# Kernel optimization log

Measured on AMD Instinct MI355X. Metric: run time of the kernel, lower is better.

Reference implementation:

```python
import jax, jax.numpy as jnp
import numpy as np


def setup_inputs() -> dict:
    key = jax.random.key(0)
    k1, k2 = jax.random.split(key)
    B, Q, K, H = 8, 2048, 2048, 128
    out_state = jax.random.normal(k1, (B, Q, H), dtype=jnp.float32)
    history = jax.random.normal(k2, (B, K, H), dtype=jnp.float32)
    return {"out_state": out_state, "history": history}


def reference(out_state, history):
    # tanh pre-activation on queries
    q = jnp.tanh(out_state)                              # [B, Q, H]
    # unscaled QK^T scores
    scores = jnp.einsum("bqh,bkh->bqk", q, history)      # [B, Q, K]
    probs = jax.nn.softmax(scores, axis=2)               # softmax over keys
    attn = jnp.einsum("bqk,bkh->bqh", probs, history)    # [B, Q, H]
    return attn
```

## Files before the change

### kernel.cpp

```cpp
#include <hip/hip_runtime.h>
#include <math.h>


typedef _Float16 half8 __attribute__((ext_vector_type(8)));
typedef _Float16 half4 __attribute__((ext_vector_type(4)));
typedef float    f32x4 __attribute__((ext_vector_type(4)));

#define QQ 2048
#define KK 2048
#define HH 128
#define BM 64
#define BN 64
#define NTILES 32
#define PS_STR 72
#define L2E 1.44269504f
#define SPLITS_TARGET 3

#define KS_STRP 136
#define VT_STRP 72

#define KH_HALVES     ((size_t)8 * KK * HH)
#define PREP_BYTES    (KH_HALVES * 4)
#define OSPLIT_BYTES  ((size_t)256 * BM * HH * 2)
#define MLSPLIT_FLOATS ((size_t)256 * BM)

union U32H { unsigned int u; _Float16 h[2]; };

typedef __attribute__((address_space(1))) const void gvoid;
typedef __attribute__((address_space(3))) void lvoid;

#define WAITVM4 asm volatile("s_waitcnt vmcnt(4)" ::: "memory")
#define WAITVM0 asm volatile("s_waitcnt vmcnt(0)" ::: "memory")
static __device__ __forceinline__ void wgbar() {
    asm volatile("" ::: "memory");
    __builtin_amdgcn_s_barrier();
    asm volatile("" ::: "memory");
}

__launch_bounds__(256)
__global__ void attn_prep(const float* __restrict__ history,
                          _Float16* __restrict__ wsh) {
    __shared__ __align__(16) _Float16 Ks[BN * KS_STRP];
    __shared__ __align__(16) _Float16 Vt[HH * VT_STRP];

    const int tid = threadIdx.x;
    const int bid = blockIdx.x;
    const int b   = bid >> 5;
    const int kt  = bid & 31;

    const float* hb = history + ((size_t)b * KK + (size_t)kt * BN) * HH;
    const int r0 = tid >> 5;
    const int c4 = (tid & 31) * 4;
    #pragma unroll
    for (int j = 0; j < 8; ++j) {
        const float4 g = *(const float4*)(hb + (size_t)(r0 + 8 * j) * HH + c4);
        half4 hv;
        hv[0] = (_Float16)g.x; hv[1] = (_Float16)g.y;
        hv[2] = (_Float16)g.z; hv[3] = (_Float16)g.w;
        *(half4*)&Ks[(r0 + 8 * j) * KS_STRP + c4] = hv;
    }
    __syncthreads();

    {
        const int h0  = 2 * (tid & 63);
        const int n0t = (tid >> 6) * 16;
        half8 ra0, ra1, rb0, rb1;
        #pragma unroll
        for (int i = 0; i < 8; ++i) {
            U32H t; t.u = *(const unsigned int*)&Ks[(n0t + i) * KS_STRP + h0];
            ra0[i] = t.h[0]; rb0[i] = t.h[1];
        }
        #pragma unroll
        for (int i = 8; i < 16; ++i) {
            U32H t; t.u = *(const unsigned int*)&Ks[(n0t + i) * KS_STRP + h0];
            ra1[i - 8] = t.h[0]; rb1[i - 8] = t.h[1];
        }
        *(half8*)&Vt[(h0    ) * VT_STRP + n0t    ] = ra0;
        *(half8*)&Vt[(h0    ) * VT_STRP + n0t + 8] = ra1;
        *(half8*)&Vt[(h0 + 1) * VT_STRP + n0t    ] = rb0;
        *(half8*)&Vt[(h0 + 1) * VT_STRP + n0t + 8] = rb1;
    }

    {
        const int k  = tid >> 2;
        const int c0 = (tid & 3) * 32;
        const int sk = (k & 7) << 3;
        _Float16* dst = wsh + ((size_t)b * KK + (size_t)kt * BN + k) * HH;
        #pragma unroll
        for (int g8 = 0; g8 < 4; ++g8)
            *(half8*)&dst[(c0 + 8 * g8) ^ sk] = *(const half8*)&Ks[k * KS_STRP + c0 + 8 * g8];
    }
    __syncthreads();

    {
        const int h  = tid >> 1;
        const int n0 = (tid & 1) * 32;
        const int th = (h & 7) << 3;
        _Float16* dst = wsh + KH_HALVES + (((size_t)b * NTILES + kt) * HH + h) * BN;
        #pragma unroll
        for (int g8 = 0; g8 < 4; ++g8)
            *(half8*)&dst[(n0 + 8 * g8) ^ th] = *(const half8*)&Vt[h * VT_STRP + n0 + 8 * g8];
    }
}

__launch_bounds__(256, 3)
__global__ void attn_main(const float* __restrict__ out_state,
                          const _Float16* __restrict__ wsh,
                          float* __restrict__ out,
                          char* __restrict__ wsb,
                          int splits) {
    __shared__ __align__(16) _Float16 Ks[BN * HH];
    __shared__ __align__(16) _Float16 Vt[HH * BN];
    __shared__ __align__(16) _Float16 Ps[4][16 * PS_STR];

    const int tid  = threadIdx.x;
    const int wave = tid >> 6;
    const int lane = tid & 63;
    const int quad = lane >> 4;
    const int lc   = lane & 15;
    const int swz  = (lc & 7) << 3;

    const int bid  = blockIdx.x;
    const int s    = bid >> 8;
    const int r256 = bid & 255;
    const int b    = r256 >> 5;
    const int qb   = r256 & 31;
    const int m0   = qb * BM;

    const int kt0 = (NTILES * s) / splits;
    const int kt1 = (NTILES * (s + 1)) / splits;

    const _Float16* khb = wsh + (size_t)b * KK * HH;
    const _Float16* vtb = wsh + KH_HALVES + (size_t)b * NTILES * (HH * BN);

    auto issueK = [&](int t) {
        const char* gsrc = (const char*)(khb + (size_t)t * (BN * HH));
        #pragma unroll
        for (int c = 0; c < 4; ++c) {
            const int off = (c * 4 + wave) * 1024 + lane * 16;
            __builtin_amdgcn_global_load_lds((gvoid*)(gsrc + off),
                                             (lvoid*)((char*)Ks + off), 16, 0, 0);
        }
    };
    auto issueV = [&](int t) {
        const char* gsrc = (const char*)(vtb + (size_t)t * (HH * BN));
        #pragma unroll
        for (int c = 0; c < 4; ++c) {
            const int off = (c * 4 + wave) * 1024 + lane * 16;
            __builtin_amdgcn_global_load_lds((gvoid*)(gsrc + off),
                                             (lvoid*)((char*)Vt + off), 16, 0, 0);
        }
    };

    issueK(kt0);
    issueV(kt0);

    half8 qf[4];
    {
        const int m = m0 + wave * 16 + lc;
        const float* qrow = out_state + ((size_t)b * QQ + m) * HH;
        float4 qa[8];
        #pragma unroll
        for (int s4 = 0; s4 < 4; ++s4) {
            qa[2 * s4]     = *(const float4*)(qrow + 32 * s4 + quad * 8);
            qa[2 * s4 + 1] = *(const float4*)(qrow + 32 * s4 + quad * 8 + 4);
        }
        #pragma unroll
        for (int s4 = 0; s4 < 4; ++s4) {
            qf[s4][0] = (_Float16)tanhf(qa[2*s4].x);   qf[s4][1] = (_Float16)tanhf(qa[2*s4].y);
            qf[s4][2] = (_Float16)tanhf(qa[2*s4].z);   qf[s4][3] = (_Float16)tanhf(qa[2*s4].w);
            qf[s4][4] = (_Float16)tanhf(qa[2*s4+1].x); qf[s4][5] = (_Float16)tanhf(qa[2*s4+1].y);
            qf[s4][6] = (_Float16)tanhf(qa[2*s4+1].z); qf[s4][7] = (_Float16)tanhf(qa[2*s4+1].w);
        }
    }

    const f32x4 zero4 = {0.f, 0.f, 0.f, 0.f};
    f32x4 O[8];
    #pragma unroll
    for (int i = 0; i < 8; ++i) O[i] = zero4;
    f32x4 Osum = zero4;
    float rmax = -3.0e38f;

    const half8 ones = {(_Float16)1.f,(_Float16)1.f,(_Float16)1.f,(_Float16)1.f,
                        (_Float16)1.f,(_Float16)1.f,(_Float16)1.f,(_Float16)1.f};

    for (int kt = kt0; kt < kt1; ++kt) {
        const bool more = (kt + 1 < kt1);

        WAITVM4;
        wgbar();

        f32x4 S[4];
        __builtin_amdgcn_s_setprio(1);
        #pragma unroll
        for (int nt = 0; nt < 4; ++nt) {
            f32x4 acc = zero4;
            #pragma unroll
            for (int s4 = 0; s4 < 4; ++s4) {
                const half8 kf = *(const half8*)
                    &Ks[((nt * 16 + lc) << 7) + ((32 * s4 + (quad << 3)) ^ swz)];
                acc = __builtin_amdgcn_mfma_f32_16x16x32_f16(kf, qf[s4], acc, 0, 0, 0);
            }
            S[nt] = acc;
        }
        __builtin_amdgcn_s_setprio(0);

        wgbar();
        if (more) issueK(kt + 1);

        float tmax = S[0][0];
        #pragma unroll
        for (int nt = 0; nt < 4; ++nt)
            #pragma unroll
            for (int r = 0; r < 4; ++r)
                tmax = fmaxf(tmax, S[nt][r]);
        tmax = fmaxf(tmax, __shfl_xor(tmax, 16, 64));
        tmax = fmaxf(tmax, __shfl_xor(tmax, 32, 64));

        if (!__all(tmax <= rmax)) {
            const float nm    = fmaxf(rmax, tmax);
            const float alpha = exp2f((rmax - nm) * L2E);
            rmax = nm;
            #pragma unroll
            for (int ct = 0; ct < 8; ++ct) O[ct] *= alpha;
            Osum *= alpha;
        }

        #pragma unroll
        for (int nt = 0; nt < 4; ++nt)
            #pragma unroll
            for (int r = 0; r < 4; ++r)
                S[nt][r] = exp2f((S[nt][r] - rmax) * L2E);

        #pragma unroll
        for (int nt = 0; nt < 4; ++nt) {
            half4 pv;
            pv[0] = (_Float16)S[nt][0]; pv[1] = (_Float16)S[nt][1];
            pv[2] = (_Float16)S[nt][2]; pv[3] = (_Float16)S[nt][3];
            *(half4*)&Ps[wave][lc * PS_STR + nt * 16 + quad * 4] = pv;
        }

        if (more) { WAITVM4; } else { WAITVM0; }
        wgbar();

        __builtin_amdgcn_s_setprio(1);
        #pragma unroll
        for (int s2 = 0; s2 < 2; ++s2) {
            const half8 pb = *(const half8*)&Ps[wave][lc * PS_STR + s2 * 32 + quad * 8];
            Osum = __builtin_amdgcn_mfma_f32_16x16x32_f16(ones, pb, Osum, 0, 0, 0);
            #pragma unroll
            for (int ct = 0; ct < 8; ++ct) {
                const half8 vf = *(const half8*)
                    &Vt[((ct * 16 + lc) << 6) + ((32 * s2 + (quad << 3)) ^ swz)];
                O[ct] = __builtin_amdgcn_mfma_f32_16x16x32_f16(vf, pb, O[ct], 0, 0, 0);
            }
        }
        __builtin_amdgcn_s_setprio(0);

        wgbar();
        if (more) issueV(kt + 1);
    }

    if (splits == 1) {
        const float inv = 1.0f / Osum[0];
        float* orow = out + ((size_t)b * QQ + m0 + wave * 16 + lc) * HH;
        #pragma unroll
        for (int ct = 0; ct < 8; ++ct) {
            f32x4 v = O[ct] * inv;
            *(f32x4*)&orow[ct * 16 + quad * 4] = v;
        }
    } else {
        const float inv = 1.0f / Osum[0];
        _Float16* oh = (_Float16*)(wsb + PREP_BYTES)
                     + ((size_t)(s * 256 + r256) * BM + wave * 16 + lc) * HH;
        #pragma unroll
        for (int ct = 0; ct < 8; ++ct) {
            const f32x4 v = O[ct] * inv;
            half4 hv;
            hv[0] = (_Float16)v[0]; hv[1] = (_Float16)v[1];
            hv[2] = (_Float16)v[2]; hv[3] = (_Float16)v[3];
            *(half4*)&oh[ct * 16 + quad * 4] = hv;
        }
        if (quad == 0) {
            float* wm = (float*)(wsb + PREP_BYTES + (size_t)splits * OSPLIT_BYTES);
            const size_t idx = (size_t)(s * 256 + r256) * BM + wave * 16 + lc;
            wm[idx] = rmax;
            wm[(size_t)splits * MLSPLIT_FLOATS + idx] = Osum[0];
        }
    }
}

__launch_bounds__(256)
__global__ void attn_combine(const char* __restrict__ wsb,
                             float* __restrict__ out,
                             int splits) {
    const int idx = blockIdx.x * 256 + threadIdx.x;
    const int h   = idx & 127;
    const int q   = (idx >> 7) & 2047;
    const int b   = idx >> 18;
    const int qb  = q >> 6;
    const int qr  = q & 63;
    const int blk = b * 32 + qb;

    const _Float16* oh = (const _Float16*)(wsb + PREP_BYTES);
    const float* wm = (const float*)(wsb + PREP_BYTES + (size_t)splits * OSPLIT_BYTES);
    const float* wl = wm + (size_t)splits * MLSPLIT_FLOATS;

    float ms[SPLITS_TARGET];
    float M = -3.0e38f;
    for (int s = 0; s < splits; ++s) {
        ms[s] = wm[(size_t)(s * 256 + blk) * BM + qr];
        M = fmaxf(M, ms[s]);
    }
    float denom = 0.f, val = 0.f;
    for (int s = 0; s < splits; ++s) {
        const float wgt = exp2f((ms[s] - M) * L2E) * wl[(size_t)(s * 256 + blk) * BM + qr];
        denom += wgt;
        val   += wgt * (float)oh[(size_t)(s * 256 + blk) * (BM * HH) + (size_t)qr * HH + h];
    }
    out[idx] = val / denom;
}

extern "C" void kernel_launch(void* const* d_in, const int* in_sizes, int n_in,
                              void* d_out, int out_size, void* d_ws, size_t ws_size,
                              hipStream_t stream) {
    const float* out_state = (const float*)d_in[0];
    const float* history   = (const float*)d_in[1];
    float* out = (float*)d_out;
    char* wsb  = (char*)d_ws;

    const size_t need3 = PREP_BYTES
                       + (size_t)SPLITS_TARGET * OSPLIT_BYTES
                       + (size_t)SPLITS_TARGET * 2 * MLSPLIT_FLOATS * 4;
    const int splits = (ws_size >= need3) ? SPLITS_TARGET : 1;

    attn_prep<<<dim3(256), dim3(256), 0, stream>>>(history, (_Float16*)wsb);
    attn_main<<<dim3(256 * splits), dim3(256), 0, stream>>>(out_state, (const _Float16*)wsb,
                                                            out, wsb, splits);
    if (splits > 1)
        attn_combine<<<dim3((8 * QQ * HH) / 256), dim3(256), 0, stream>>>(wsb, out, splits);
}
```

Before: 120.9 us.

## Switch attention to 32x32 MFMA with register-resident P and four splits

The main kernel moves from 16x16x32 to 32x32x16 MFMA tiles with 2 waves per block, each wave owning 32 query rows. P now stays in registers and is rearranged with cross-half shuffles rather than going through LDS, and the row sum is accumulated with scalar adds instead of a ones-MFMA. tanh and exp use fast hardware exp2/rcp intrinsics. The prep kernel swizzles in LDS and writes coalesced. Splits go to 4 when the workspace allows, and the combine kernel is templated and vectorised. The cost is larger per-thread register pressure and fewer threads per block.

Result: faster. 108.5 us (-10.3%).

```diff
diff --git a/kernel.cpp b/kernel.cpp
--- a/kernel.cpp
+++ b/kernel.cpp
@@ -2,9 +2,12 @@
 #include <math.h>
 
 
-typedef _Float16 half8 __attribute__((ext_vector_type(8)));
-typedef _Float16 half4 __attribute__((ext_vector_type(4)));
-typedef float    f32x4 __attribute__((ext_vector_type(4)));
+typedef _Float16 half8  __attribute__((ext_vector_type(8)));
+typedef _Float16 half4  __attribute__((ext_vector_type(4)));
+typedef __fp16   fp16x2 __attribute__((ext_vector_type(2)));
+typedef float    f32x4  __attribute__((ext_vector_type(4)));
+typedef float    f32x2  __attribute__((ext_vector_type(2)));
+typedef float    f32x16 __attribute__((ext_vector_type(16)));
 
 #define QQ 2048
 #define KK 2048
@@ -12,24 +15,21 @@
 #define BM 64
 #define BN 64
 #define NTILES 32
-#define PS_STR 72
 #define L2E 1.44269504f
-#define SPLITS_TARGET 3
-
-#define KS_STRP 136
-#define VT_STRP 72
-
-#define KH_HALVES     ((size_t)8 * KK * HH)
-#define PREP_BYTES    (KH_HALVES * 4)
-#define OSPLIT_BYTES  ((size_t)256 * BM * HH * 2)
+
+#define KH_HALVES      ((size_t)8 * KK * HH)
+#define PREP_BYTES     (KH_HALVES * 4)
+#define OSPLIT_BYTES   ((size_t)256 * BM * HH * 2)
 #define MLSPLIT_FLOATS ((size_t)256 * BM)
 
 union U32H { unsigned int u; _Float16 h[2]; };
+union H2I  { fp16x2 h; int i; };
+union I4H8 { int i[4]; half8 h; };
 
 typedef __attribute__((address_space(1))) const void gvoid;
 typedef __attribute__((address_space(3))) void lvoid;
 
-#define WAITVM4 asm volatile("s_waitcnt vmcnt(4)" ::: "memory")
+#define WAITVM8 asm volatile("s_waitcnt vmcnt(8)" ::: "memory")
 #define WAITVM0 asm volatile("s_waitcnt vmcnt(0)" ::: "memory")
 static __device__ __forceinline__ void wgbar() {
     asm volatile("" ::: "memory");
@@ -38,10 +38,10 @@
 }
 
 __launch_bounds__(256)
-__global__ void attn_prep(const float* __restrict__ history,
-                          _Float16* __restrict__ wsh) {
-    __shared__ __align__(16) _Float16 Ks[BN * KS_STRP];
-    __shared__ __align__(16) _Float16 Vt[HH * VT_STRP];
+__global__ void attn_prep_k(const float* __restrict__ history,
+                            _Float16* __restrict__ wsh) {
+    __shared__ __align__(16) _Float16 Ks[BN * HH];
+    __shared__ __align__(16) _Float16 Vt[HH * BN];
 
     const int tid = threadIdx.x;
     const int bid = blockIdx.x;
@@ -53,11 +53,12 @@
     const int c4 = (tid & 31) * 4;
     #pragma unroll
     for (int j = 0; j < 8; ++j) {
-        const float4 g = *(const float4*)(hb + (size_t)(r0 + 8 * j) * HH + c4);
+        const int k = r0 + 8 * j;
+        const float4 g = *(const float4*)(hb + (size_t)k * HH + c4);
         half4 hv;
         hv[0] = (_Float16)g.x; hv[1] = (_Float16)g.y;
         hv[2] = (_Float16)g.z; hv[3] = (_Float16)g.w;
-        *(half4*)&Ks[(r0 + 8 * j) * KS_STRP + c4] = hv;
+        *(half4*)&Ks[k * HH + (c4 ^ ((k & 7) << 3))] = hv;
     }
     __syncthreads();
 
@@ -67,65 +68,58 @@
         half8 ra0, ra1, rb0, rb1;
         #pragma unroll
         for (int i = 0; i < 8; ++i) {
-            U32H t; t.u = *(const unsigned int*)&Ks[(n0t + i) * KS_STRP + h0];
+            const int n = n0t + i;
+            U32H t; t.u = *(const unsigned int*)&Ks[n * HH + (h0 ^ ((n & 7) << 3))];
             ra0[i] = t.h[0]; rb0[i] = t.h[1];
         }
         #pragma unroll
         for (int i = 8; i < 16; ++i) {
-            U32H t; t.u = *(const unsigned int*)&Ks[(n0t + i) * KS_STRP + h0];
+            const int n = n0t + i;
+            U32H t; t.u = *(const unsigned int*)&Ks[n * HH + (h0 ^ ((n & 7) << 3))];
             ra1[i - 8] = t.h[0]; rb1[i - 8] = t.h[1];
         }
-        *(half8*)&Vt[(h0    ) * VT_STRP + n0t    ] = ra0;
-        *(half8*)&Vt[(h0    ) * VT_STRP + n0t + 8] = ra1;
-        *(half8*)&Vt[(h0 + 1) * VT_STRP + n0t    ] = rb0;
-        *(half8*)&Vt[(h0 + 1) * VT_STRP + n0t + 8] = rb1;
-    }
-
-    {
-        const int k  = tid >> 2;
-        const int c0 = (tid & 3) * 32;
-        const int sk = (k & 7) << 3;
-        _Float16* dst = wsh + ((size_t)b * KK + (size_t)kt * BN + k) * HH;
-        #pragma unroll
-        for (int g8 = 0; g8 < 4; ++g8)
-            *(half8*)&dst[(c0 + 8 * g8) ^ sk] = *(const half8*)&Ks[k * KS_STRP + c0 + 8 * g8];
+        const int th0 = (h0 & 7) << 3;
+        const int th1 = ((h0 + 1) & 7) << 3;
+        *(half8*)&Vt[(h0    ) * BN + ((n0t    ) ^ th0)] = ra0;
+        *(half8*)&Vt[(h0    ) * BN + ((n0t + 8) ^ th0)] = ra1;
+        *(half8*)&Vt[(h0 + 1) * BN + ((n0t    ) ^ th1)] = rb0;
+        *(half8*)&Vt[(h0 + 1) * BN + ((n0t + 8) ^ th1)] = rb1;
     }
     __syncthreads();
 
-    {
-        const int h  = tid >> 1;
-        const int n0 = (tid & 1) * 32;
-        const int th = (h & 7) << 3;
-        _Float16* dst = wsh + KH_HALVES + (((size_t)b * NTILES + kt) * HH + h) * BN;
-        #pragma unroll
-        for (int g8 = 0; g8 < 4; ++g8)
-            *(half8*)&dst[(n0 + 8 * g8) ^ th] = *(const half8*)&Vt[h * VT_STRP + n0 + 8 * g8];
-    }
-}
-
-__launch_bounds__(256, 3)
-__global__ void attn_main(const float* __restrict__ out_state,
-                          const _Float16* __restrict__ wsh,
-                          float* __restrict__ out,
-                          char* __restrict__ wsb,
-                          int splits) {
-    __shared__ __align__(16) _Float16 Ks[BN * HH];
-    __shared__ __align__(16) _Float16 Vt[HH * BN];
-    __shared__ __align__(16) _Float16 Ps[4][16 * PS_STR];
+    _Float16* kdst = wsh + ((size_t)b * KK + (size_t)kt * BN) * HH;
+    _Float16* vdst = wsh + KH_HALVES + ((size_t)(b * NTILES + kt)) * (HH * BN);
+    const f32x4* ksrc = (const f32x4*)Ks;
+    const f32x4* vsrc = (const f32x4*)Vt;
+    #pragma unroll
+    for (int i = 0; i < 4; ++i) {
+        ((f32x4*)kdst)[i * 256 + tid] = ksrc[i * 256 + tid];
+        ((f32x4*)vdst)[i * 256 + tid] = vsrc[i * 256 + tid];
+    }
+}
+
+__launch_bounds__(128, 2)
+__global__ void attn_main_k(const float* __restrict__ out_state,
+                            const _Float16* __restrict__ wsh,
+                            float* __restrict__ out,
+                            char* __restrict__ wsb,
+                            int splits) {
+    __shared__ __align__(16) _Float16 KsL[BN * HH];
+    __shared__ __align__(16) _Float16 VtL[HH * BN];
 
     const int tid  = threadIdx.x;
     const int wave = tid >> 6;
     const int lane = tid & 63;
-    const int quad = lane >> 4;
-    const int lc   = lane & 15;
-    const int swz  = (lc & 7) << 3;
+    const int l31  = lane & 31;
+    const int hi   = lane >> 5;
+    const int swzk = (lane & 7) << 3;
 
     const int bid  = blockIdx.x;
     const int s    = bid >> 8;
     const int r256 = bid & 255;
     const int b    = r256 >> 5;
     const int qb   = r256 & 31;
-    const int m0   = qb * BM;
+    const int q    = qb * BM + wave * 32 + l31;
 
     const int kt0 = (NTILES * s) / splits;
     const int kt1 = (NTILES * (s + 1)) / splits;
@@ -134,125 +128,142 @@
     const _Float16* vtb = wsh + KH_HALVES + (size_t)b * NTILES * (HH * BN);
 
     auto issueK = [&](int t) {
-        const char* gsrc = (const char*)(khb + (size_t)t * (BN * HH));
-        #pragma unroll
-        for (int c = 0; c < 4; ++c) {
-            const int off = (c * 4 + wave) * 1024 + lane * 16;
-            __builtin_amdgcn_global_load_lds((gvoid*)(gsrc + off),
-                                             (lvoid*)((char*)Ks + off), 16, 0, 0);
+        const char* g = (const char*)(khb + (size_t)t * (BN * HH));
+        #pragma unroll
+        for (int c = 0; c < 8; ++c) {
+            const int off = (c * 2 + wave) * 1024 + lane * 16;
+            __builtin_amdgcn_global_load_lds((gvoid*)(g + off),
+                                             (lvoid*)((char*)KsL + off), 16, 0, 0);
         }
     };
     auto issueV = [&](int t) {
-        const char* gsrc = (const char*)(vtb + (size_t)t * (HH * BN));
-        #pragma unroll
-        for (int c = 0; c < 4; ++c) {
-            const int off = (c * 4 + wave) * 1024 + lane * 16;
-            __builtin_amdgcn_global_load_lds((gvoid*)(gsrc + off),
-                                             (lvoid*)((char*)Vt + off), 16, 0, 0);
+        const char* g = (const char*)(vtb + (size_t)t * (HH * BN));
+        #pragma unroll
+        for (int c = 0; c < 8; ++c) {
+            const int off = (c * 2 + wave) * 1024 + lane * 16;
+            __builtin_amdgcn_global_load_lds((gvoid*)(g + off),
+                                             (lvoid*)((char*)VtL + off), 16, 0, 0);
         }
     };
 
+    float4 qa[16];
+    {
+        const float* qrow = out_state + ((size_t)b * QQ + q) * HH;
+        #pragma unroll
+        for (int hs = 0; hs < 8; ++hs) {
+            qa[2 * hs]     = *(const float4*)(qrow + hs * 16 + hi * 8);
+            qa[2 * hs + 1] = *(const float4*)(qrow + hs * 16 + hi * 8 + 4);
+        }
+    }
     issueK(kt0);
     issueV(kt0);
 
-    half8 qf[4];
-    {
-        const int m = m0 + wave * 16 + lc;
-        const float* qrow = out_state + ((size_t)b * QQ + m) * HH;
-        float4 qa[8];
-        #pragma unroll
-        for (int s4 = 0; s4 < 4; ++s4) {
-            qa[2 * s4]     = *(const float4*)(qrow + 32 * s4 + quad * 8);
-            qa[2 * s4 + 1] = *(const float4*)(qrow + 32 * s4 + quad * 8 + 4);
-        }
-        #pragma unroll
-        for (int s4 = 0; s4 < 4; ++s4) {
-            qf[s4][0] = (_Float16)tanhf(qa[2*s4].x);   qf[s4][1] = (_Float16)tanhf(qa[2*s4].y);
-            qf[s4][2] = (_Float16)tanhf(qa[2*s4].z);   qf[s4][3] = (_Float16)tanhf(qa[2*s4].w);
-            qf[s4][4] = (_Float16)tanhf(qa[2*s4+1].x); qf[s4][5] = (_Float16)tanhf(qa[2*s4+1].y);
-            qf[s4][6] = (_Float16)tanhf(qa[2*s4+1].z); qf[s4][7] = (_Float16)tanhf(qa[2*s4+1].w);
-        }
-    }
-
-    const f32x4 zero4 = {0.f, 0.f, 0.f, 0.f};
-    f32x4 O[8];
-    #pragma unroll
-    for (int i = 0; i < 8; ++i) O[i] = zero4;
-    f32x4 Osum = zero4;
+    auto th = [](float x) {
+        const float e = __builtin_amdgcn_exp2f(x * (2.0f * L2E));
+        return 1.0f - 2.0f * __builtin_amdgcn_rcpf(e + 1.0f);
+    };
+    half8 qf[8];
+    #pragma unroll
+    for (int hs = 0; hs < 8; ++hs) {
+        const float4 a = qa[2 * hs], c = qa[2 * hs + 1];
+        qf[hs][0] = (_Float16)th(a.x); qf[hs][1] = (_Float16)th(a.y);
+        qf[hs][2] = (_Float16)th(a.z); qf[hs][3] = (_Float16)th(a.w);
+        qf[hs][4] = (_Float16)th(c.x); qf[hs][5] = (_Float16)th(c.y);
+        qf[hs][6] = (_Float16)th(c.z); qf[hs][7] = (_Float16)th(c.w);
+    }
+
+    f32x16 O[4];
+    #pragma unroll
+    for (int i = 0; i < 4; ++i)
+        #pragma unroll
+        for (int r = 0; r < 16; ++r) O[i][r] = 0.f;
+    float Osum = 0.f;
     float rmax = -3.0e38f;
-
-    const half8 ones = {(_Float16)1.f,(_Float16)1.f,(_Float16)1.f,(_Float16)1.f,
-                        (_Float16)1.f,(_Float16)1.f,(_Float16)1.f,(_Float16)1.f};
 
     for (int kt = kt0; kt < kt1; ++kt) {
         const bool more = (kt + 1 < kt1);
 
-        WAITVM4;
+        WAITVM8;
         wgbar();
 
-        f32x4 S[4];
+        f32x16 S0, S1;
+        #pragma unroll
+        for (int r = 0; r < 16; ++r) { S0[r] = 0.f; S1[r] = 0.f; }
         __builtin_amdgcn_s_setprio(1);
         #pragma unroll
-        for (int nt = 0; nt < 4; ++nt) {
-            f32x4 acc = zero4;
-            #pragma unroll
-            for (int s4 = 0; s4 < 4; ++s4) {
-                const half8 kf = *(const half8*)
-                    &Ks[((nt * 16 + lc) << 7) + ((32 * s4 + (quad << 3)) ^ swz)];
-                acc = __builtin_amdgcn_mfma_f32_16x16x32_f16(kf, qf[s4], acc, 0, 0, 0);
-            }
-            S[nt] = acc;
+        for (int hs = 0; hs < 8; ++hs) {
+            const int col = (hs * 16 + hi * 8) ^ swzk;
+            const half8 k0 = *(const half8*)&KsL[l31 * 128 + col];
+            const half8 k1 = *(const half8*)&KsL[(l31 + 32) * 128 + col];
+            S0 = __builtin_amdgcn_mfma_f32_32x32x16_f16(k0, qf[hs], S0, 0, 0, 0);
+            S1 = __builtin_amdgcn_mfma_f32_32x32x16_f16(k1, qf[hs], S1, 0, 0, 0);
         }
         __builtin_amdgcn_s_setprio(0);
 
         wgbar();
         if (more) issueK(kt + 1);
 
-        float tmax = S[0][0];
-        #pragma unroll
-        for (int nt = 0; nt < 4; ++nt)
-            #pragma unroll
-            for (int r = 0; r < 4; ++r)
-                tmax = fmaxf(tmax, S[nt][r]);
-        tmax = fmaxf(tmax, __shfl_xor(tmax, 16, 64));
+        float tmax = S0[0];
+        #pragma unroll
+        for (int r = 1; r < 16; ++r) tmax = fmaxf(tmax, S0[r]);
+        #pragma unroll
+        for (int r = 0; r < 16; ++r) tmax = fmaxf(tmax, S1[r]);
         tmax = fmaxf(tmax, __shfl_xor(tmax, 32, 64));
 
         if (!__all(tmax <= rmax)) {
             const float nm    = fmaxf(rmax, tmax);
-            const float alpha = exp2f((rmax - nm) * L2E);
+            const float alpha = __builtin_amdgcn_exp2f((rmax - nm) * L2E);
             rmax = nm;
             #pragma unroll
-            for (int ct = 0; ct < 8; ++ct) O[ct] *= alpha;
+            for (int i = 0; i < 4; ++i) O[i] *= alpha;
             Osum *= alpha;
         }
 
         #pragma unroll
-        for (int nt = 0; nt < 4; ++nt)
+        for (int r = 0; r < 16; ++r) S0[r] = __builtin_amdgcn_exp2f((S0[r] - rmax) * L2E);
+        #pragma unroll
+        for (int r = 0; r < 16; ++r) S1[r] = __builtin_amdgcn_exp2f((S1[r] - rmax) * L2E);
+
+        float ls = 0.f;
+        #pragma unroll
+        for (int r = 0; r < 16; ++r) ls += S0[r] + S1[r];
+        Osum += ls + __shfl_xor(ls, 32, 64);
+
+        int d0[8], d1[8];
+        #pragma unroll
+        for (int M = 0; M < 8; ++M) {
+            const int r0 = (M & 3) * 4;
+            H2I u0, u1;
+            if (M < 4) {
+                u0.h = __builtin_amdgcn_cvt_pkrtz(S0[r0], S0[r0 + 1]);
+                u1.h = __builtin_amdgcn_cvt_pkrtz(S0[r0 + 2], S0[r0 + 3]);
+            } else {
+                u0.h = __builtin_amdgcn_cvt_pkrtz(S1[r0], S1[r0 + 1]);
+                u1.h = __builtin_amdgcn_cvt_pkrtz(S1[r0 + 2], S1[r0 + 3]);
+            }
+            d0[M] = u0.i; d1[M] = u1.i;
+        }
+
+        if (more) { WAITVM8; } else { WAITVM0; }
+        wgbar();
+
+        __builtin_amdgcn_s_setprio(1);
+        #pragma unroll
+        for (int ns = 0; ns < 4; ++ns) {
+            const int x  = d0[2 * ns],     x2 = d1[2 * ns];
+            const int y  = d0[2 * ns + 1], y2 = d1[2 * ns + 1];
+            const int px  = __shfl_xor(x, 32, 64),  px2 = __shfl_xor(x2, 32, 64);
+            const int py  = __shfl_xor(y, 32, 64),  py2 = __shfl_xor(y2, 32, 64);
+            I4H8 bf;
+            bf.i[0] = hi ? py  : x;
+            bf.i[1] = hi ? py2 : x2;
+            bf.i[2] = hi ? y   : px;
+            bf.i[3] = hi ? y2  : px2;
             #pragma unroll
-            for (int r = 0; r < 4; ++r)
-                S[nt][r] = exp2f((S[nt][r] - rmax) * L2E);
-
-        #pragma unroll
-        for (int nt = 0; nt < 4; ++nt) {
-            half4 pv;
-            pv[0] = (_Float16)S[nt][0]; pv[1] = (_Float16)S[nt][1];
-            pv[2] = (_Float16)S[nt][2]; pv[3] = (_Float16)S[nt][3];
-            *(half4*)&Ps[wave][lc * PS_STR + nt * 16 + quad * 4] = pv;
-        }
-
-        if (more) { WAITVM4; } else { WAITVM0; }
-        wgbar();
-
-        __builtin_amdgcn_s_setprio(1);
-        #pragma unroll
-        for (int s2 = 0; s2 < 2; ++s2) {
-            const half8 pb = *(const half8*)&Ps[wave][lc * PS_STR + s2 * 32 + quad * 8];
-            Osum = __builtin_amdgcn_mfma_f32_16x16x32_f16(ones, pb, Osum, 0, 0, 0);
-            #pragma unroll
-            for (int ct = 0; ct < 8; ++ct) {
+            for (int ht = 0; ht < 4; ++ht) {
                 const half8 vf = *(const half8*)
-                    &Vt[((ct * 16 + lc) << 6) + ((32 * s2 + (quad << 3)) ^ swz)];
-                O[ct] = __builtin_amdgcn_mfma_f32_16x16x32_f16(vf, pb, O[ct], 0, 0, 0);
+                    &VtL[(ht * 32 + l31) * 64 + ((ns * 16 + hi * 8) ^ swzk)];
+                O[ht] = __builtin_amdgcn_mfma_f32_32x32x16_f16(vf, bf.h, O[ht], 0, 0, 0);
             }
         }
         __builtin_amdgcn_s_setprio(0);
@@ -262,63 +273,77 @@
     }
 
     if (splits == 1) {
-        const float inv = 1.0f / Osum[0];
-        float* orow = out + ((size_t)b * QQ + m0 + wave * 16 + lc) * HH;
-        #pragma unroll
-        for (int ct = 0; ct < 8; ++ct) {
-            f32x4 v = O[ct] * inv;
-            *(f32x4*)&orow[ct * 16 + quad * 4] = v;
-        }
+        const float inv = 1.0f / Osum;
+        float* orow = out + ((size_t)b * QQ + q) * HH;
+        #pragma unroll
+        for (int ht = 0; ht < 4; ++ht)
+            #pragma unroll
+            for (int m = 0; m < 4; ++m) {
+                f32x4 v;
+                v[0] = O[ht][4 * m]     * inv; v[1] = O[ht][4 * m + 1] * inv;
+                v[2] = O[ht][4 * m + 2] * inv; v[3] = O[ht][4 * m + 3] * inv;
+                *(f32x4*)&orow[ht * 32 + 8 * m + 4 * hi] = v;
+            }
     } else {
-        const float inv = 1.0f / Osum[0];
+        const float inv = 1.0f / Osum;
         _Float16* oh = (_Float16*)(wsb + PREP_BYTES)
-                     + ((size_t)(s * 256 + r256) * BM + wave * 16 + lc) * HH;
-        #pragma unroll
-        for (int ct = 0; ct < 8; ++ct) {
-            const f32x4 v = O[ct] * inv;
-            half4 hv;
-            hv[0] = (_Float16)v[0]; hv[1] = (_Float16)v[1];
-            hv[2] = (_Float16)v[2]; hv[3] = (_Float16)v[3];
-            *(half4*)&oh[ct * 16 + quad * 4] = hv;
-        }
-        if (quad == 0) {
+                     + ((size_t)(s * 256 + r256) * BM + wave * 32 + l31) * HH;
+        #pragma unroll
+        for (int ht = 0; ht < 4; ++ht)
+            #pragma unroll
+            for (int m = 0; m < 4; ++m) {
+                half4 hv;
+                hv[0] = (_Float16)(O[ht][4 * m]     * inv);
+                hv[1] = (_Float16)(O[ht][4 * m + 1] * inv);
+                hv[2] = (_Float16)(O[ht][4 * m + 2] * inv);
+                hv[3] = (_Float16)(O[ht][4 * m + 3] * inv);
+                *(half4*)&oh[ht * 32 + 8 * m + 4 * hi] = hv;
+            }
+        if (!hi) {
             float* wm = (float*)(wsb + PREP_BYTES + (size_t)splits * OSPLIT_BYTES);
-            const size_t idx = (size_t)(s * 256 + r256) * BM + wave * 16 + lc;
+            const size_t idx = (size_t)(s * 256 + r256) * BM + wave * 32 + l31;
             wm[idx] = rmax;
-            wm[(size_t)splits * MLSPLIT_FLOATS + idx] = Osum[0];
-        }
-    }
-}
-
+            wm[(size_t)splits * MLSPLIT_FLOATS + idx] = Osum;
+        }
+    }
+}
+
+template<int SPL>
 __launch_bounds__(256)
-__global__ void attn_combine(const char* __restrict__ wsb,
-                             float* __restrict__ out,
-                             int splits) {
+__global__ void attn_combine_k(const char* __restrict__ wsb,
+                               float* __restrict__ out) {
     const int idx = blockIdx.x * 256 + threadIdx.x;
-    const int h   = idx & 127;
-    const int q   = (idx >> 7) & 2047;
-    const int b   = idx >> 18;
-    const int qb  = q >> 6;
+    const int h2  = idx & 63;
+    const int q   = (idx >> 6) & 2047;
+    const int b   = idx >> 17;
+    const int blk = b * 32 + (q >> 6);
     const int qr  = q & 63;
-    const int blk = b * 32 + qb;
 
     const _Float16* oh = (const _Float16*)(wsb + PREP_BYTES);
-    const float* wm = (const float*)(wsb + PREP_BYTES + (size_t)splits * OSPLIT_BYTES);
-    const float* wl = wm + (size_t)splits * MLSPLIT_FLOATS;
-
-    float ms[SPLITS_TARGET];
+    const float* wm = (const float*)(wsb + PREP_BYTES + (size_t)SPL * OSPLIT_BYTES);
+    const float* wl = wm + (size_t)SPL * MLSPLIT_FLOATS;
+
+    float ms[SPL];
     float M = -3.0e38f;
-    for (int s = 0; s < splits; ++s) {
+    #pragma unroll
+    for (int s = 0; s < SPL; ++s) {
         ms[s] = wm[(size_t)(s * 256 + blk) * BM + qr];
         M = fmaxf(M, ms[s]);
     }
-    float denom = 0.f, val = 0.f;
-    for (int s = 0; s < splits; ++s) {
+    float denom = 0.f, v0 = 0.f, v1 = 0.f;
+    #pragma unroll
+    for (int s = 0; s < SPL; ++s) {
         const float wgt = exp2f((ms[s] - M) * L2E) * wl[(size_t)(s * 256 + blk) * BM + qr];
         denom += wgt;
-        val   += wgt * (float)oh[(size_t)(s * 256 + blk) * (BM * HH) + (size_t)qr * HH + h];
-    }
-    out[idx] = val / denom;
+        U32H t;
+        t.u = *(const unsigned int*)&oh[(size_t)(s * 256 + blk) * (BM * HH)
+                                        + (size_t)qr * HH + 2 * h2];
+        v0 += wgt * (float)t.h[0];
+        v1 += wgt * (float)t.h[1];
+    }
+    const float inv = 1.0f / denom;
+    f32x2 r; r[0] = v0 * inv; r[1] = v1 * inv;
+    *(f32x2*)&out[((size_t)(b * QQ + q)) * HH + 2 * h2] = r;
 }
 
 extern "C" void kernel_launch(void* const* d_in, const int* in_sizes, int n_in,
@@ -329,14 +354,15 @@
     float* out = (float*)d_out;
     char* wsb  = (char*)d_ws;
 
-    const size_t need3 = PREP_BYTES
-                       + (size_t)SPLITS_TARGET * OSPLIT_BYTES
-                       + (size_t)SPLITS_TARGET * 2 * MLSPLIT_FLOATS * 4;
-    const int splits = (ws_size >= need3) ? SPLITS_TARGET : 1;
-
-    attn_prep<<<dim3(256), dim3(256), 0, stream>>>(history, (_Float16*)wsb);
-    attn_main<<<dim3(256 * splits), dim3(256), 0, stream>>>(out_state, (const _Float16*)wsb,
-                                                            out, wsb, splits);
-    if (splits > 1)
-        attn_combine<<<dim3((8 * QQ * HH) / 256), dim3(256), 0, stream>>>(wsb, out, splits);
-}
+    const size_t need4 = PREP_BYTES + 4 * OSPLIT_BYTES + 4 * 2 * MLSPLIT_FLOATS * 4;
+    const size_t need3 = PREP_BYTES + 3 * OSPLIT_BYTES + 3 * 2 * MLSPLIT_FLOATS * 4;
+    const int splits = (ws_size >= need4) ? 4 : (ws_size >= need3) ? 3 : 1;
+
+    attn_prep_k<<<dim3(256), dim3(256), 0, stream>>>(history, (_Float16*)wsb);
+    attn_main_k<<<dim3(256 * splits), dim3(128), 0, stream>>>(out_state, (const _Float16*)wsb,
+                                                              out, wsb, splits);
+    if (splits == 4)
+        attn_combine_k<4><<<dim3(4096), dim3(256), 0, stream>>>(wsb, out);
+    else if (splits == 3)
+        attn_combine_k<3><<<dim3(4096), dim3(256), 0, stream>>>(wsb, out);
+}
```
